# Kernel optimization log

Measured on AMD Instinct MI355X. Metric: run time of the kernel, lower is better.

Reference implementation:

```python
import jax, jax.numpy as jnp
import numpy as np

CONF_W, POS_W, LEN_W, TRIG_W, CONST_W = 1.0, 1.0, 0.1, 1.0, 0.5
FOCAL_THR = 0.1
EPS = 6e-08


def setup_inputs() -> dict:
    key = jax.random.key(0)
    k1, k2, k3, k4, k5 = jax.random.split(key, 5)
    B, C, H, W = 32, 10, 192, 320
    u = jax.random.uniform(k1, (B, H, W), dtype=jnp.float32)
    gt0 = jnp.where(u > 0.95, 1.0, u * 2.0 - 1.0)
    gt_rest = jax.random.normal(k2, (B, C - 1, H, W), dtype=jnp.float32) * 0.5
    gt = jnp.concatenate([gt0[:, None], gt_rest], axis=1)
    # re channel 0: confidence strictly in (0,1) so logs are finite
    re0 = jax.random.uniform(k3, (B, 1, H, W), dtype=jnp.float32, minval=0.05, maxval=0.95)
    re_rest = jax.random.normal(k4, (B, C - 1, H, W), dtype=jnp.float32) * 0.5
    re = jnp.concatenate([re0, re_rest], axis=1)
    return {"re": re, "gt": gt}


def _smooth_l1(d):
    ad = jnp.abs(d)
    return jnp.where(ad < 1.0, 0.5 * d * d, ad - 0.5)


def _forward(re, gt):
    gt0 = gt[:, 0]  # [B,H,W]
    re0 = re[:, 0]
    m0 = gt0 >= 0.0            # confidence mask (above 0)
    mv = gt0 == 1.0            # vehicle mask
    m0f = m0.astype(jnp.float32)
    mvf = mv.astype(jnp.float32)
    nv = mvf.sum()             # number of vehicle pixels (one channel)

    def mse2(rc, gc):
        # mean over two masked channels
        s = sum(((re[:, r] - gt[:, g]) ** 2 * mvf).sum() for r, g in zip(rc, gc))
        return s / (2.0 * nv)

    def sl1_2(rc, gc):
        s = sum((_smooth_l1(re[:, r] - gt[:, g]) * mvf).sum() for r, g in zip(rc, gc))
        return s / (2.0 * nv)

    # focal confidence loss (threshold 0.1) over pixels with gt0 >= 0
    pos = m0f * (gt0 >= FOCAL_THR).astype(jnp.float32)
    neg = m0f * (gt0 < FOCAL_THR).astype(jnp.float32)
    num_pos = pos.sum()
    safe_re = jnp.clip(re0, 1e-6, 1.0 - 1e-6)  # masked-out entries must not NaN
    pos_term = -(pos * (gt0 - re0) ** 2 * jnp.log(safe_re + EPS)).sum()
    neg_term = -(neg * re0 ** 2 * jnp.log(1.0 + EPS - safe_re) * (1.0 - gt0) ** 4).sum()
    focal = jnp.where(num_pos == 0.0, neg_term, (pos_term + neg_term) / num_pos)

    confidence_loss = CONF_W * focal
    pos_loss = POS_W * sl1_2([1, 2], [1, 2])
    length_v1 = LEN_W * sl1_2([3, 6], [3, 6])
    length_v2 = LEN_W * sl1_2([3, 6], [6, 3])
    trig_v1 = TRIG_W * (mse2([4, 7], [4, 7]) + mse2([5, 8], [5, 8]))
    trig_v2 = TRIG_W * (mse2([4, 7], [7, 4]) + mse2([5, 8], [8, 5]))

    const1 = (((1.0 - re[:, 5] ** 2 - re[:, 4] ** 2) ** 2) * mvf).sum() / nv
    const2 = (((1.0 - re[:, 8] ** 2 - re[:, 7] ** 2) ** 2) * mvf).sum() / nv
    const_loss = CONST_W * (const1 + const2)

    height_loss = LEN_W * (_smooth_l1(re[:, 9] - gt[:, 9]) * mvf).sum() / nv

    dimensions_loss = jnp.minimum(length_v1 + trig_v1, length_v2 + trig_v2) + height_loss
    return confidence_loss + pos_loss + dimensions_loss + const_loss


def reference(re, gt):
    return _forward(re, gt)
```

## Files before the change

kernel.cpp:

```cpp
#include <hip/hip_runtime.h>
#include <math.h>

constexpr int B_ = 32, C_ = 10, H_ = 192, W_ = 320;
constexpr int HW_  = H_ * W_;
constexpr int CHW_ = C_ * HW_;
constexpr int NPTS = B_ * HW_;
constexpr int PPT  = 4;
constexpr int TPB  = 128;
constexpr int NTHR = NPTS / PPT;
constexpr int NBLK = NTHR / TPB;

#define NACC 7

__device__ __forceinline__ float sl1f(float d) {
    float ad = fabsf(d);
    return ad < 1.0f ? 0.5f * d * d : ad - 0.5f;
}

__global__ __launch_bounds__(TPB) void loss_main(
    const float* __restrict__ re, const float* __restrict__ gt,
    float* __restrict__ ws)
{
    const int tid = blockIdx.x * TPB + threadIdx.x;
    const int p = tid * PPT;
    const int b = p / HW_;
    const int s = p - b * HW_;
    const float* rp = re + (size_t)b * CHW_ + s;
    const float* gp = gt + (size_t)b * CHW_ + s;

    float4 R[10], G[10];
#pragma unroll
    for (int c = 0; c < 10; ++c) {
        R[c] = *(const float4*)(rp + c * HW_);
        G[c] = *(const float4*)(gp + c * HW_);
    }
    __builtin_amdgcn_sched_barrier(0);

    float acc[NACC];
#pragma unroll
    for (int i = 0; i < NACC; ++i) acc[i] = 0.0f;

#pragma unroll
    for (int j = 0; j < PPT; ++j) {
        #define RC(c) (((const float*)&R[c])[j])
        #define GC(c) (((const float*)&G[c])[j])
        const float g = GC(0), r = RC(0);
        const float m = (g == 1.0f) ? 1.0f : 0.0f;
        acc[0] += m;
        const float pos = (g >= 0.1f) ? 1.0f : 0.0f;
        const float neg = ((g >= 0.0f) && (g < 0.1f)) ? 1.0f : 0.0f;
        acc[1] += pos;
        const float safe = fminf(fmaxf(r, 1e-6f), 1.0f - 1e-6f);
        const float larg = (pos != 0.0f) ? (safe + 6e-8f)
                                         : (1.0f + 6e-8f - safe);
        const float lg = logf(larg);
        const float d0 = g - r;
        acc[2] += pos * (d0 * d0) * lg;
        const float omg = 1.0f - g;
        const float omg2 = omg * omg;
        acc[3] += neg * (r * r) * (omg2 * omg2) * lg;

        const float r1 = RC(1), r2 = RC(2), r3 = RC(3), r4v = RC(4);
        const float r5 = RC(5), r6 = RC(6), r7 = RC(7), r8 = RC(8), r9 = RC(9);
        const float g1 = GC(1), g2 = GC(2), g3 = GC(3), g4v = GC(4);
        const float g5 = GC(5), g6 = GC(6), g7 = GC(7), g8 = GC(8), g9 = GC(9);

        const float sp = sl1f(r1 - g1) + sl1f(r2 - g2);
        const float c1 = 1.0f - r5 * r5 - r4v * r4v;
        const float c2 = 1.0f - r8 * r8 - r7 * r7;
        const float sc = c1 * c1 + c2 * c2;
        const float sh = sl1f(r9 - g9);
        acc[4] += m * (0.5f * sp + 0.5f * sc + 0.1f * sh);

        const float d44 = r4v - g4v, d77 = r7 - g7;
        const float d55 = r5 - g5,  d88 = r8 - g8;
        const float t1 = d44 * d44 + d77 * d77 + d55 * d55 + d88 * d88;
        const float l1 = sl1f(r3 - g3) + sl1f(r6 - g6);
        acc[5] += m * (0.05f * l1 + 0.5f * t1);

        const float d47 = r4v - g7, d74 = r7 - g4v;
        const float d58 = r5 - g8,  d85 = r8 - g5;
        const float t2 = d47 * d47 + d74 * d74 + d58 * d58 + d85 * d85;
        const float l2 = sl1f(r3 - g6) + sl1f(r6 - g3);
        acc[6] += m * (0.05f * l2 + 0.5f * t2);
        #undef RC
        #undef GC
    }

    __shared__ float smem[NACC][2];
    const int lane = threadIdx.x & 63;
    const int wid  = threadIdx.x >> 6;
#pragma unroll
    for (int i = 0; i < NACC; ++i) {
        float v = acc[i];
#pragma unroll
        for (int off = 32; off > 0; off >>= 1) v += __shfl_down(v, off, 64);
        if (lane == 0) smem[i][wid] = v;
    }
    __syncthreads();
    if (threadIdx.x < NACC) {
        const int i = threadIdx.x;
        ws[i * NBLK + blockIdx.x] = smem[i][0] + smem[i][1];
    }
}

__global__ __launch_bounds__(1024) void loss_reduce(
    const float* __restrict__ ws, float* __restrict__ out)
{
    float acc[NACC];
#pragma unroll
    for (int i = 0; i < NACC; ++i) acc[i] = 0.0f;

#pragma unroll
    for (int k = 0; k < 4; ++k) {
        const int idx = threadIdx.x + k * 1024;
        if (idx < NBLK) {
#pragma unroll
            for (int i = 0; i < NACC; ++i)
                acc[i] += ws[i * NBLK + idx];
        }
    }

    __shared__ float smem[NACC][16];
    const int lane = threadIdx.x & 63;
    const int wid  = threadIdx.x >> 6;
#pragma unroll
    for (int i = 0; i < NACC; ++i) {
        float v = acc[i];
#pragma unroll
        for (int off = 32; off > 0; off >>= 1) v += __shfl_down(v, off, 64);
        if (lane == 0) smem[i][wid] = v;
    }
    __syncthreads();

    if (threadIdx.x == 0) {
        float slot[NACC];
#pragma unroll
        for (int i = 0; i < NACC; ++i) {
            float v = 0.0f;
#pragma unroll
            for (int w = 0; w < 16; ++w) v += smem[i][w];
            slot[i] = v;
        }
        const float nv    = slot[0];
        const float npos  = slot[1];
        const float pterm = -slot[2];
        const float nterm = -slot[3];
        const float focal = (npos == 0.0f) ? nterm : (pterm + nterm) / npos;
        out[0] = focal + (slot[4] + fminf(slot[5], slot[6])) / nv;
    }
}

extern "C" void kernel_launch(void* const* d_in, const int* in_sizes, int n_in,
                              void* d_out, int out_size, void* d_ws, size_t ws_size,
                              hipStream_t stream)
{
    const float* re = (const float*)d_in[0];
    const float* gt = (const float*)d_in[1];
    float* ws  = (float*)d_ws;
    float* out = (float*)d_out;

    loss_main<<<NBLK, TPB, 0, stream>>>(re, gt, ws);
    loss_reduce<<<1, 1024, 0, stream>>>(ws, out);
}
```

Before: 175.7 us.

## Double-buffer float2 loads across multiple tiles per block

Each block now processes six tiles of float2 points per thread, issuing loads for the next tile while computing on the current one (ping-pong register buffers). This is meant to hide global memory latency and keep more bytes in flight per thread over time. The grid shrinks to a third, and the final reduce kernel is resized to 640 threads to match. Fewer blocks may reduce latency hiding via occupancy, and float2 loads are narrower than the previous float4 loads.

```diff
diff --git a/kernel.cpp b/kernel.cpp
--- a/kernel.cpp
+++ b/kernel.cpp
@@ -5,10 +5,13 @@
 constexpr int HW_  = H_ * W_;
 constexpr int CHW_ = C_ * HW_;
 constexpr int NPTS = B_ * HW_;
-constexpr int PPT  = 4;
-constexpr int TPB  = 128;
-constexpr int NTHR = NPTS / PPT;
-constexpr int NBLK = NTHR / TPB;
+
+constexpr int TPB   = 128;
+constexpr int PPT   = 2;
+constexpr int TILES = 6;
+constexpr int TPTS  = TPB * PPT;
+constexpr int BSPAN = TPTS * TILES;
+constexpr int NBLK  = NPTS / BSPAN;
 
 #define NACC 7
 
@@ -21,71 +24,95 @@
     const float* __restrict__ re, const float* __restrict__ gt,
     float* __restrict__ ws)
 {
-    const int tid = blockIdx.x * TPB + threadIdx.x;
-    const int p = tid * PPT;
-    const int b = p / HW_;
-    const int s = p - b * HW_;
-    const float* rp = re + (size_t)b * CHW_ + s;
-    const float* gp = gt + (size_t)b * CHW_ + s;
-
-    float4 R[10], G[10];
-#pragma unroll
-    for (int c = 0; c < 10; ++c) {
-        R[c] = *(const float4*)(rp + c * HW_);
-        G[c] = *(const float4*)(gp + c * HW_);
-    }
-    __builtin_amdgcn_sched_barrier(0);
+    const int p0 = blockIdx.x * BSPAN + threadIdx.x * PPT;
+    const int b  = p0 / HW_;
+    const int s0 = p0 - b * HW_;
+    const float* rp = re + (size_t)b * CHW_ + s0;
+    const float* gp = gt + (size_t)b * CHW_ + s0;
 
     float acc[NACC];
 #pragma unroll
     for (int i = 0; i < NACC; ++i) acc[i] = 0.0f;
 
-#pragma unroll
-    for (int j = 0; j < PPT; ++j) {
-        #define RC(c) (((const float*)&R[c])[j])
-        #define GC(c) (((const float*)&G[c])[j])
-        const float g = GC(0), r = RC(0);
-        const float m = (g == 1.0f) ? 1.0f : 0.0f;
-        acc[0] += m;
-        const float pos = (g >= 0.1f) ? 1.0f : 0.0f;
-        const float neg = ((g >= 0.0f) && (g < 0.1f)) ? 1.0f : 0.0f;
-        acc[1] += pos;
-        const float safe = fminf(fmaxf(r, 1e-6f), 1.0f - 1e-6f);
-        const float larg = (pos != 0.0f) ? (safe + 6e-8f)
-                                         : (1.0f + 6e-8f - safe);
-        const float lg = logf(larg);
-        const float d0 = g - r;
-        acc[2] += pos * (d0 * d0) * lg;
-        const float omg = 1.0f - g;
-        const float omg2 = omg * omg;
-        acc[3] += neg * (r * r) * (omg2 * omg2) * lg;
+    float2 RA[10], GA[10], RB[10], GB[10];
 
-        const float r1 = RC(1), r2 = RC(2), r3 = RC(3), r4v = RC(4);
-        const float r5 = RC(5), r6 = RC(6), r7 = RC(7), r8 = RC(8), r9 = RC(9);
-        const float g1 = GC(1), g2 = GC(2), g3 = GC(3), g4v = GC(4);
-        const float g5 = GC(5), g6 = GC(6), g7 = GC(7), g8 = GC(8), g9 = GC(9);
+#define ISSUE(Rb_, Gb_, OFF) do {                                         \
+        _Pragma("unroll")                                                 \
+        for (int c = 0; c < 10; ++c) {                                    \
+            Rb_[c] = *(const float2*)(rp + c * HW_ + (OFF));              \
+            Gb_[c] = *(const float2*)(gp + c * HW_ + (OFF));              \
+        }                                                                 \
+    } while (0)
 
-        const float sp = sl1f(r1 - g1) + sl1f(r2 - g2);
-        const float c1 = 1.0f - r5 * r5 - r4v * r4v;
-        const float c2 = 1.0f - r8 * r8 - r7 * r7;
-        const float sc = c1 * c1 + c2 * c2;
-        const float sh = sl1f(r9 - g9);
-        acc[4] += m * (0.5f * sp + 0.5f * sc + 0.1f * sh);
+#define COMPUTE(Rb_, Gb_) do {                                            \
+        _Pragma("unroll")                                                 \
+        for (int j = 0; j < PPT; ++j) {                                   \
+            const float g = ((const float*)&Gb_[0])[j];                   \
+            const float r = ((const float*)&Rb_[0])[j];                   \
+            const float m = (g == 1.0f) ? 1.0f : 0.0f;                    \
+            acc[0] += m;                                                  \
+            const float pos = (g >= 0.1f) ? 1.0f : 0.0f;                  \
+            const float neg = ((g >= 0.0f) && (g < 0.1f)) ? 1.0f : 0.0f;  \
+            acc[1] += pos;                                                \
+            const float safe = fminf(fmaxf(r, 1e-6f), 1.0f - 1e-6f);      \
+            const float larg = (pos != 0.0f) ? (safe + 6e-8f)             \
+                                             : (1.0f + 6e-8f - safe);     \
+            const float lg = logf(larg);                                  \
+            const float d0 = g - r;                                       \
+            acc[2] += pos * (d0 * d0) * lg;                               \
+            const float omg = 1.0f - g;                                   \
+            const float omg2 = omg * omg;                                 \
+            acc[3] += neg * (r * r) * (omg2 * omg2) * lg;                 \
+            const float r1 = ((const float*)&Rb_[1])[j];                  \
+            const float r2 = ((const float*)&Rb_[2])[j];                  \
+            const float r3 = ((const float*)&Rb_[3])[j];                  \
+            const float r4v = ((const float*)&Rb_[4])[j];                 \
+            const float r5 = ((const float*)&Rb_[5])[j];                  \
+            const float r6 = ((const float*)&Rb_[6])[j];                  \
+            const float r7 = ((const float*)&Rb_[7])[j];                  \
+            const float r8 = ((const float*)&Rb_[8])[j];                  \
+            const float r9 = ((const float*)&Rb_[9])[j];                  \
+            const float g1 = ((const float*)&Gb_[1])[j];                  \
+            const float g2 = ((const float*)&Gb_[2])[j];                  \
+            const float g3 = ((const float*)&Gb_[3])[j];                  \
+            const float g4v = ((const float*)&Gb_[4])[j];                 \
+            const float g5 = ((const float*)&Gb_[5])[j];                  \
+            const float g6 = ((const float*)&Gb_[6])[j];                  \
+            const float g7 = ((const float*)&Gb_[7])[j];                  \
+            const float g8 = ((const float*)&Gb_[8])[j];                  \
+            const float g9 = ((const float*)&Gb_[9])[j];                  \
+            const float sp = sl1f(r1 - g1) + sl1f(r2 - g2);               \
+            const float c1 = 1.0f - r5 * r5 - r4v * r4v;                  \
+            const float c2 = 1.0f - r8 * r8 - r7 * r7;                    \
+            const float sc = c1 * c1 + c2 * c2;                           \
+            const float sh = sl1f(r9 - g9);                               \
+            acc[4] += m * (0.5f * sp + 0.5f * sc + 0.1f * sh);            \
+            const float d44 = r4v - g4v, d77 = r7 - g7;                   \
+            const float d55 = r5 - g5,  d88 = r8 - g8;                    \
+            const float t1 = d44*d44 + d77*d77 + d55*d55 + d88*d88;       \
+            const float l1 = sl1f(r3 - g3) + sl1f(r6 - g6);               \
+            acc[5] += m * (0.05f * l1 + 0.5f * t1);                       \
+            const float d47 = r4v - g7, d74 = r7 - g4v;                   \
+            const float d58 = r5 - g8,  d85 = r8 - g5;                    \
+            const float t2 = d47*d47 + d74*d74 + d58*d58 + d85*d85;       \
+            const float l2 = sl1f(r3 - g6) + sl1f(r6 - g3);               \
+            acc[6] += m * (0.05f * l2 + 0.5f * t2);                       \
+        }                                                                 \
+    } while (0)
 
-        const float d44 = r4v - g4v, d77 = r7 - g7;
-        const float d55 = r5 - g5,  d88 = r8 - g8;
-        const float t1 = d44 * d44 + d77 * d77 + d55 * d55 + d88 * d88;
-        const float l1 = sl1f(r3 - g3) + sl1f(r6 - g6);
-        acc[5] += m * (0.05f * l1 + 0.5f * t1);
+    ISSUE(RA, GA, 0);
 
-        const float d47 = r4v - g7, d74 = r7 - g4v;
-        const float d58 = r5 - g8,  d85 = r8 - g5;
-        const float t2 = d47 * d47 + d74 * d74 + d58 * d58 + d85 * d85;
-        const float l2 = sl1f(r3 - g6) + sl1f(r6 - g3);
-        acc[6] += m * (0.05f * l2 + 0.5f * t2);
-        #undef RC
-        #undef GC
+#pragma unroll 1
+    for (int k = 0; k < TILES / 2; ++k) {
+        const int toff = k * (2 * TPTS);
+        ISSUE(RB, GB, toff + TPTS);
+        COMPUTE(RA, GA);
+        if (k + 1 < TILES / 2)
+            ISSUE(RA, GA, toff + 2 * TPTS);
+        COMPUTE(RB, GB);
     }
+#undef ISSUE
+#undef COMPUTE
 
     __shared__ float smem[NACC][2];
     const int lane = threadIdx.x & 63;
@@ -104,7 +131,7 @@
     }
 }
 
-__global__ __launch_bounds__(1024) void loss_reduce(
+__global__ __launch_bounds__(640) void loss_reduce(
     const float* __restrict__ ws, float* __restrict__ out)
 {
     float acc[NACC];
@@ -112,16 +139,14 @@
     for (int i = 0; i < NACC; ++i) acc[i] = 0.0f;
 
 #pragma unroll
-    for (int k = 0; k < 4; ++k) {
-        const int idx = threadIdx.x + k * 1024;
-        if (idx < NBLK) {
+    for (int k = 0; k < 2; ++k) {
+        const int idx = threadIdx.x + k * 640;
 #pragma unroll
-            for (int i = 0; i < NACC; ++i)
-                acc[i] += ws[i * NBLK + idx];
-        }
+        for (int i = 0; i < NACC; ++i)
+            acc[i] += ws[i * NBLK + idx];
     }
 
-    __shared__ float smem[NACC][16];
+    __shared__ float smem[NACC][10];
     const int lane = threadIdx.x & 63;
     const int wid  = threadIdx.x >> 6;
 #pragma unroll
@@ -139,7 +164,7 @@
         for (int i = 0; i < NACC; ++i) {
             float v = 0.0f;
 #pragma unroll
-            for (int w = 0; w < 16; ++w) v += smem[i][w];
+            for (int w = 0; w < 10; ++w) v += smem[i][w];
             slot[i] = v;
         }
         const float nv    = slot[0];
@@ -161,5 +186,5 @@
     float* out = (float*)d_out;
 
     loss_main<<<NBLK, TPB, 0, stream>>>(re, gt, ws);
-    loss_reduce<<<1, 1024, 0, stream>>>(ws, out);
+    loss_reduce<<<1, 640, 0, stream>>>(ws, out);
 }
```

After: 179.5 us. 1.02x slower.
